# Kernel optimization log

Hardware: AMD Instinct MI355X
Metric: run time of the kernel (lower is better)

## Reference

```python
import jax, jax.numpy as jnp
import numpy as np

# Config matching init_kwargs: N=4 networks, dims 128 -> 1024 -> 1024 -> 512
A, B, D = 8, 2048, 128     # agents, batch, input size
N = 4                       # number of independent SePS networks
H1, H2, H3 = 1024, 1024, 512


def setup_inputs() -> dict:
    key = jax.random.key(0)
    ks = jax.random.split(key, 6)
    inputs = jax.random.normal(ks[0], (A, B, D), dtype=jnp.float32)  # stacked per-agent obs
    seps_indices = jax.random.randint(ks[1], (B, A), 0, N)           # cluster id per (sample, agent)
    scale = lambda k, shape, fan: jax.random.normal(k, shape, dtype=jnp.float32) * (1.0 / np.sqrt(fan))
    W0 = scale(ks[2], (N, D, H1), D);   b0 = jnp.zeros((N, H1), jnp.float32)
    W1 = scale(ks[3], (N, H1, H2), H1); b1 = jnp.zeros((N, H2), jnp.float32)
    W2 = scale(ks[4], (N, H2, H3), H2); b2 = jnp.zeros((N, H3), jnp.float32)
    return {"inputs": inputs, "seps_indices": seps_indices,
            "W0": W0, "b0": b0, "W1": W1, "b1": b1, "W2": W2, "b2": b2}


def reference(inputs, seps_indices, W0, b0, W1, b1, W2, b2):
    # Run every network densely on the full stacked input, as the torch module does.
    # inputs: [A, B, D]; W*: [N, in, out]
    h = jax.nn.relu(jnp.einsum('abd,ndh->nabh', inputs, W0) + b0[:, None, None, :])
    h = jax.nn.relu(jnp.einsum('nabh,nhk->nabk', h, W1) + b1[:, None, None, :])
    out_all = jnp.einsum('nabk,nko->nabo', h, W2) + b2[:, None, None, :]  # [N, A, B, H3]
    # Gather along the network axis per (agent, sample): seps_indices is [B, A]
    idx = seps_indices.T                              # [A, B]
    a = jnp.arange(inputs.shape[0])[:, None]          # [A, 1]
    b = jnp.arange(inputs.shape[1])[None, :]          # [1, B]
    return out_all[idx, a, b, :]                      # [A, B, H3] (stacked per-agent outputs)
```

## Files before the change

### kernel.cpp

```cpp
#include <hip/hip_runtime.h>
#include <hip/hip_bf16.h>

#define AG 8
#define BT 2048
#define RT (AG*BT)
#define NNET 4
#define D0 128
#define H1 1024
#define H2 1024
#define H3 512

#define XBLK 40

typedef __attribute__((ext_vector_type(8))) short short8;
typedef __attribute__((ext_vector_type(4))) float f32x4;

__device__ __forceinline__ unsigned short f2bf(float f){
  unsigned int x = __float_as_uint(f);
  x += 0x7fff + ((x >> 16) & 1);
  return (unsigned short)(x >> 16);
}

__device__ __forceinline__ void gload_lds16(const void* g, void* l){
  __builtin_amdgcn_global_load_lds(
      (const __attribute__((address_space(1))) unsigned int*)g,
      (__attribute__((address_space(3))) unsigned int*)l, 16, 0, 0);
}

__device__ __forceinline__ int bucket_off(const int* counts, int n){
  int s = 0;
  #pragma unroll
  for (int i = 0; i < NNET-1; i++) if (i < n) s += counts[i];
  return s;
}

__global__ void k_init(int* counts){
  if (threadIdx.x < NNET) counts[threadIdx.x] = 0;
}

__global__ __launch_bounds__(256) void k_compact(const int* __restrict__ seps,
                          int* __restrict__ counts, int* __restrict__ rowlist){
  __shared__ int lcount[NNET];
  __shared__ int lbase[NNET];
  int t = blockIdx.x * 256 + threadIdx.x;
  if (threadIdx.x < NNET) lcount[threadIdx.x] = 0;
  __syncthreads();
  int a = t >> 11, b = t & (BT-1);
  int n = seps[b*AG + a];
  int lrank = atomicAdd(&lcount[n], 1);
  __syncthreads();
  if (threadIdx.x < NNET)
    lbase[threadIdx.x] = atomicAdd(&counts[threadIdx.x], lcount[threadIdx.x]);
  __syncthreads();
  rowlist[n*RT + lbase[n] + lrank] = t;
}

template<int K, int NOUT>
__global__ __launch_bounds__(256) void k_transpose(const float* __restrict__ W,
                                                   unsigned short* __restrict__ WT){
  __shared__ float tile[32][33];
  int n = blockIdx.z;
  int k0 = blockIdx.x*32, o0 = blockIdx.y*32;
  const float* Wn = W + (size_t)n*K*NOUT;
  unsigned short* WTn = WT + (size_t)n*NOUT*K;
  int tx = threadIdx.x & 31, ty0 = threadIdx.x >> 5;
  #pragma unroll
  for (int r = 0; r < 32; r += 8)
    tile[ty0 + r][tx] = Wn[(size_t)(k0 + ty0 + r)*NOUT + o0 + tx];
  __syncthreads();
  #pragma unroll
  for (int r = 0; r < 32; r += 8)
    WTn[(size_t)(o0 + ty0 + r)*K + k0 + tx] = f2bf(tile[tx][ty0 + r]);
}

__global__ __launch_bounds__(256) void k_gather0(const float* __restrict__ X,
                          const int* __restrict__ counts,
                          const int* __restrict__ rowlist, unsigned short* __restrict__ X0h){
  int n = blockIdx.y;
  int cnt = counts[n];
  int i = blockIdx.x*16 + (threadIdx.x >> 4);
  if (i >= cnt) return;
  int off = bucket_off(counts, n);
  int orig = rowlist[n*RT + i];
  int c = (threadIdx.x & 15) * 8;
  const float* src = X + (size_t)orig*D0 + c;
  float4 v0 = *(const float4*)src, v1 = *(const float4*)(src+4);
  ushort4 u0, u1;
  u0.x=f2bf(v0.x); u0.y=f2bf(v0.y); u0.z=f2bf(v0.z); u0.w=f2bf(v0.w);
  u1.x=f2bf(v1.x); u1.y=f2bf(v1.y); u1.z=f2bf(v1.z); u1.w=f2bf(v1.w);
  unsigned short* dst = X0h + (size_t)(off + i)*D0 + c;
  *(ushort4*)dst = u0; *(ushort4*)(dst+4) = u1;
}

template<int K, int NOUT, int RELU, int SCATTER>
__global__ __launch_bounds__(256, 4) void k_mlp(
    const unsigned short* __restrict__ X,
    const unsigned short* __restrict__ WT,
    const float* __restrict__ Bias,
    const int* __restrict__ counts,
    const int* __restrict__ rowlist,
    unsigned short* __restrict__ Yh,
    float* __restrict__ Yf)
{
  constexpr int T = K / 32;
  const int n = blockIdx.z;
  const int cnt = counts[n];
  const int i0 = blockIdx.x * 128;
  if (i0 >= cnt) return;
  const int off = bucket_off(counts, n);
  const int bn = blockIdx.y * 128;

  __shared__ __align__(16) unsigned short As[2][128*32];
  __shared__ __align__(16) unsigned short Bs[2][128*32];
  __shared__ int rs[128];

  const int t = threadIdx.x, lane = t & 63, wave = t >> 6;
  const int wm = wave >> 1, wn = wave & 1;
  const int lr = lane & 15, g = lane >> 4;

  if (SCATTER && t < 128) rs[t] = rowlist[n*RT + min(i0 + t, cnt-1)];

  const unsigned short* pA[2]; const unsigned short* pB[2];
  unsigned int ldsoff[2];
  const unsigned short* WTn = WT + (size_t)n * NOUT * K;
  #pragma unroll
  for (int j = 0; j < 2; j++){
    int r  = (j*4 + wave)*16 + (lane >> 2);
    int ps = lane & 3;
    int ls = ps ^ ((r >> 1) & 3);
    int rA = min(i0 + r, cnt-1);
    pA[j] = X   + (size_t)(off + rA)*K + ls*8;
    pB[j] = WTn + (size_t)(bn  + r )*K + ls*8;
    ldsoff[j] = (unsigned)(j*4 + wave) * 512;
  }

  int aoff[4], boff[4];
  #pragma unroll
  for (int i = 0; i < 4; i++){
    int ra = wm*64 + i*16 + lr;
    aoff[i] = ra*32 + (g ^ ((ra>>1)&3))*8;
    int rb = wn*64 + i*16 + lr;
    boff[i] = rb*32 + (g ^ ((rb>>1)&3))*8;
  }

  __syncthreads();

  #pragma unroll
  for (int j = 0; j < 2; j++){
    gload_lds16(pA[j], &As[0][ldsoff[j]]);
    gload_lds16(pB[j], &Bs[0][ldsoff[j]]);
    pA[j] += 32; pB[j] += 32;
  }

  f32x4 acc[4][4] = {};
  for (int ks = 0; ks < T; ++ks){
    const int b = ks & 1;
    asm volatile("s_waitcnt vmcnt(0)" ::: "memory");
    asm volatile("s_waitcnt lgkmcnt(0)" ::: "memory");
    __builtin_amdgcn_s_barrier();
    __builtin_amdgcn_sched_barrier(0);

    if (ks + 1 < T){
      #pragma unroll
      for (int j = 0; j < 2; j++){
        gload_lds16(pA[j], &As[b^1][ldsoff[j]]);
        gload_lds16(pB[j], &Bs[b^1][ldsoff[j]]);
        pA[j] += 32; pB[j] += 32;
      }
    }

    short8 av[4], bv[4];
    #pragma unroll
    for (int i = 0; i < 4; i++) av[i] = *(const short8*)&As[b][aoff[i]];
    #pragma unroll
    for (int i = 0; i < 4; i++) bv[i] = *(const short8*)&Bs[b][boff[i]];
    #pragma unroll
    for (int mi = 0; mi < 4; mi++)
      #pragma unroll
      for (int ni = 0; ni < 4; ni++)
        acc[mi][ni] = __builtin_amdgcn_mfma_f32_16x16x32_bf16(bv[ni], av[mi], acc[mi][ni], 0, 0, 0);
  }

  f32x4 bias4[4];
  #pragma unroll
  for (int ni = 0; ni < 4; ni++)
    bias4[ni] = *(const f32x4*)&Bias[n*NOUT + bn + wn*64 + ni*16 + (g<<2)];

  #pragma unroll
  for (int mi = 0; mi < 4; mi++){
    int rloc = wm*64 + mi*16 + lr;
    int grow = i0 + rloc;
    if (grow < cnt){
      #pragma unroll
      for (int ni = 0; ni < 4; ni++){
        float o[4];
        #pragma unroll
        for (int i = 0; i < 4; i++){
          float v = acc[mi][ni][i] + bias4[ni][i];
          if (RELU) v = fmaxf(v, 0.f);
          o[i] = v;
        }
        int cb = bn + wn*64 + ni*16 + (g<<2);
        if (SCATTER){
          *(float4*)&Yf[(size_t)rs[rloc]*NOUT + cb] = make_float4(o[0],o[1],o[2],o[3]);
        } else {
          ushort4 u;
          u.x=f2bf(o[0]); u.y=f2bf(o[1]); u.z=f2bf(o[2]); u.w=f2bf(o[3]);
          *(ushort4*)&Yh[(size_t)(off + grow)*NOUT + cb] = u;
        }
      }
    }
  }
}

extern "C" void kernel_launch(void* const* d_in, const int* in_sizes, int n_in,
                              void* d_out, int out_size, void* d_ws, size_t ws_size,
                              hipStream_t stream) {
  const float* inputs = (const float*)d_in[0];
  const int*   seps   = (const int*)  d_in[1];
  const float* W0     = (const float*)d_in[2];
  const float* b0     = (const float*)d_in[3];
  const float* W1     = (const float*)d_in[4];
  const float* b1     = (const float*)d_in[5];
  const float* W2     = (const float*)d_in[6];
  const float* b2     = (const float*)d_in[7];
  float* out = (float*)d_out;

  char* ws = (char*)d_ws;
  int* counts  = (int*)ws;
  int* rowlist = (int*)(ws + 4096);
  const size_t MB = 1u << 20;
  unsigned short* WT0 = (unsigned short*)(ws + 1*MB);
  unsigned short* WT1 = (unsigned short*)(ws + 2*MB);
  unsigned short* WT2 = (unsigned short*)(ws + 10*MB);
  unsigned short* h1  = (unsigned short*)(ws + 14*MB);
  unsigned short* h2  = (unsigned short*)(ws + 46*MB);
  unsigned short* X0h = (unsigned short*)(ws + 46*MB);

  k_init   <<<1, 64, 0, stream>>>(counts);
  k_compact<<<RT/256, 256, 0, stream>>>(seps, counts, rowlist);

  k_transpose<D0, H1><<<dim3(D0/32, H1/32, NNET), 256, 0, stream>>>(W0, WT0);
  k_transpose<H1, H2><<<dim3(H1/32, H2/32, NNET), 256, 0, stream>>>(W1, WT1);
  k_transpose<H2, H3><<<dim3(H2/32, H3/32, NNET), 256, 0, stream>>>(W2, WT2);
  k_gather0<<<dim3(RT/16, NNET), 256, 0, stream>>>(inputs, counts, rowlist, X0h);

  k_mlp<D0, H1, 1, 0><<<dim3(XBLK, H1/128, NNET), 256, 0, stream>>>(
      X0h, WT0, b0, counts, rowlist, h1, nullptr);
  k_mlp<H1, H2, 1, 0><<<dim3(XBLK, H2/128, NNET), 256, 0, stream>>>(
      h1, WT1, b1, counts, rowlist, h2, nullptr);
  k_mlp<H2, H3, 0, 1><<<dim3(XBLK, H3/128, NNET), 256, 0, stream>>>(
      h2, WT2, b2, counts, rowlist, nullptr, out);
}
```

Measured before the change: 142.2 us.

## Load weight fragments directly into registers instead of staging through LDS

The B (weight) operand tile is no longer staged in shared memory. Each wave now loads its own short8 weight fragments straight from global memory into registers, double-buffered one k-step ahead. This removes the B LDS buffers and their LDS reads. In exchange, weight rows are now read redundantly by the two waves that share a column half, the global loads are strided per lane, and register pressure rises, so the occupancy hint is lowered from 4 to 3.

```diff
diff --git a/kernel.cpp b/kernel.cpp
--- a/kernel.cpp
+++ b/kernel.cpp
@@ -93,7 +93,7 @@
 }
 
 template<int K, int NOUT, int RELU, int SCATTER>
-__global__ __launch_bounds__(256, 4) void k_mlp(
+__global__ __launch_bounds__(256, 3) void k_mlp(
     const unsigned short* __restrict__ X,
     const unsigned short* __restrict__ WT,
     const float* __restrict__ Bias,
@@ -111,7 +111,6 @@
   const int bn = blockIdx.y * 128;
 
   __shared__ __align__(16) unsigned short As[2][128*32];
-  __shared__ __align__(16) unsigned short Bs[2][128*32];
   __shared__ int rs[128];
 
   const int t = threadIdx.x, lane = t & 63, wave = t >> 6;
@@ -120,37 +119,41 @@
 
   if (SCATTER && t < 128) rs[t] = rowlist[n*RT + min(i0 + t, cnt-1)];
 
-  const unsigned short* pA[2]; const unsigned short* pB[2];
-  unsigned int ldsoff[2];
-  const unsigned short* WTn = WT + (size_t)n * NOUT * K;
+  const unsigned short* pA[2];
+  unsigned int ldsoffA[2];
   #pragma unroll
   for (int j = 0; j < 2; j++){
     int r  = (j*4 + wave)*16 + (lane >> 2);
     int ps = lane & 3;
     int ls = ps ^ ((r >> 1) & 3);
     int rA = min(i0 + r, cnt-1);
-    pA[j] = X   + (size_t)(off + rA)*K + ls*8;
-    pB[j] = WTn + (size_t)(bn  + r )*K + ls*8;
-    ldsoff[j] = (unsigned)(j*4 + wave) * 512;
-  }
-
-  int aoff[4], boff[4];
+    pA[j] = X + (size_t)(off + rA)*K + ls*8;
+    ldsoffA[j] = (unsigned)(j*4 + wave) * 512;
+  }
+
+  int aoff[4];
   #pragma unroll
   for (int i = 0; i < 4; i++){
     int ra = wm*64 + i*16 + lr;
     aoff[i] = ra*32 + (g ^ ((ra>>1)&3))*8;
-    int rb = wn*64 + i*16 + lr;
-    boff[i] = rb*32 + (g ^ ((rb>>1)&3))*8;
-  }
+  }
+
+  const unsigned short* WTn = WT + (size_t)n * NOUT * K;
+  const unsigned short* pb[4];
+  #pragma unroll
+  for (int i = 0; i < 4; i++)
+    pb[i] = WTn + (size_t)(bn + wn*64 + i*16 + lr)*K + g*8;
 
   __syncthreads();
 
   #pragma unroll
   for (int j = 0; j < 2; j++){
-    gload_lds16(pA[j], &As[0][ldsoff[j]]);
-    gload_lds16(pB[j], &Bs[0][ldsoff[j]]);
-    pA[j] += 32; pB[j] += 32;
-  }
+    gload_lds16(pA[j], &As[0][ldsoffA[j]]);
+    pA[j] += 32;
+  }
+  short8 bcur[4], bnxt[4];
+  #pragma unroll
+  for (int i = 0; i < 4; i++){ bnxt[i] = *(const short8*)pb[i]; pb[i] += 32; }
 
   f32x4 acc[4][4] = {};
   for (int ks = 0; ks < T; ++ks){
@@ -160,25 +163,27 @@
     __builtin_amdgcn_s_barrier();
     __builtin_amdgcn_sched_barrier(0);
 
+    #pragma unroll
+    for (int i = 0; i < 4; i++) bcur[i] = bnxt[i];
+
     if (ks + 1 < T){
       #pragma unroll
       for (int j = 0; j < 2; j++){
-        gload_lds16(pA[j], &As[b^1][ldsoff[j]]);
-        gload_lds16(pB[j], &Bs[b^1][ldsoff[j]]);
-        pA[j] += 32; pB[j] += 32;
+        gload_lds16(pA[j], &As[b^1][ldsoffA[j]]);
+        pA[j] += 32;
       }
+      #pragma unroll
+      for (int i = 0; i < 4; i++){ bnxt[i] = *(const short8*)pb[i]; pb[i] += 32; }
     }
 
-    short8 av[4], bv[4];
+    short8 av[4];
     #pragma unroll
     for (int i = 0; i < 4; i++) av[i] = *(const short8*)&As[b][aoff[i]];
     #pragma unroll
-    for (int i = 0; i < 4; i++) bv[i] = *(const short8*)&Bs[b][boff[i]];
-    #pragma unroll
     for (int mi = 0; mi < 4; mi++)
       #pragma unroll
       for (int ni = 0; ni < 4; ni++)
-        acc[mi][ni] = __builtin_amdgcn_mfma_f32_16x16x32_bf16(bv[ni], av[mi], acc[mi][ni], 0, 0, 0);
+        acc[mi][ni] = __builtin_amdgcn_mfma_f32_16x16x32_bf16(bcur[ni], av[mi], acc[mi][ni], 0, 0, 0);
   }
 
   f32x4 bias4[4];
```

Measured after the change: 201.6 us. 41.8% more time.
